# Performance work log

Hardware: AMD Instinct MI355X
Metric: run time of the kernel (lower is better)

The kernel has to match this reference:

```python
import jax, jax.numpy as jnp
import numpy as np

V, D, T, H, L, B = 50257, 1024, 1024, 16, 6, 2
HS = D // H  # 64
EPS = 1e-5


def setup_inputs() -> dict:
    key = jax.random.key(0)
    ks = jax.random.split(key, 16)
    s = 0.02
    n = lambda k, sh: jax.random.normal(k, sh, jnp.float32) * s
    return {
        'idx': jax.random.randint(ks[0], (B, T), 0, V),
        'targets': jax.random.randint(ks[1], (B, T), 0, V),
        'tok_emb': n(ks[2], (V, D)),
        'pos_emb': n(ks[3], (T, D)),
        'wq': n(ks[4], (L, H, D, HS)),
        'wk': n(ks[5], (L, H, D, HS)),
        'wv': n(ks[6], (L, H, D, HS)),
        'wproj': n(ks[7], (L, D, D)),
        'bproj': jnp.zeros((L, D), jnp.float32),
        'ln1_g': jnp.ones((L, D), jnp.float32),
        'ln1_b': jnp.zeros((L, D), jnp.float32),
        'ln2_g': jnp.ones((L, D), jnp.float32),
        'ln2_b': jnp.zeros((L, D), jnp.float32),
        'w1': n(ks[8], (L, D, 4 * D)),
        'b1': jnp.zeros((L, 4 * D), jnp.float32),
        'w2': n(ks[9], (L, 4 * D, D)),
        'b2': jnp.zeros((L, D), jnp.float32),
        'lnf_g': jnp.ones((D,), jnp.float32),
        'lnf_b': jnp.zeros((D,), jnp.float32),
        'lm_w': n(ks[10], (D, V)),
        'lm_b': jnp.zeros((V,), jnp.float32),
    }


def _layernorm(x, g, b):
    mu = jnp.mean(x, axis=-1, keepdims=True)
    var = jnp.var(x, axis=-1, keepdims=True)
    return (x - mu) * jax.lax.rsqrt(var + EPS) * g + b


def _forward(idx, targets, tok_emb, pos_emb, wq, wk, wv, wproj, bproj,
             ln1_g, ln1_b, ln2_g, ln2_b, w1, b1, w2, b2, lnf_g, lnf_b, lm_w, lm_b):
    t = idx.shape[1]
    x = tok_emb[idx] + pos_emb[:t]  # [B,T,D]
    causal = jnp.tril(jnp.ones((t, t), bool))  # [T,T]
    neg_inf = jnp.float32(-jnp.inf)

    def block(x, p):
        (wq_l, wk_l, wv_l, wp_l, bp_l, g1, b1_ln, g2, b2_ln, wf1, bf1, wf2, bf2) = p
        h = _layernorm(x, g1, b1_ln)
        q = jnp.einsum('btd,hdk->bhtk', h, wq_l)
        k = jnp.einsum('btd,hdk->bhtk', h, wk_l)
        v = jnp.einsum('btd,hdk->bhtk', h, wv_l)
        scores = jnp.einsum('bhtk,bhsk->bhts', q, k) * (HS ** -0.5)
        scores = jnp.where(causal, scores, neg_inf)
        attn = jax.nn.softmax(scores, axis=-1)  # dropout p=0.0
        o = jnp.einsum('bhts,bhsk->bhtk', attn, v)
        o = o.transpose(0, 2, 1, 3).reshape(x.shape[0], t, H * HS)  # concat heads
        x = x + o @ wp_l + bp_l
        h2 = _layernorm(x, g2, b2_ln)
        x = x + jax.nn.relu(h2 @ wf1 + bf1) @ wf2 + bf2
        return x, None

    x, _ = jax.lax.scan(block, x, (wq, wk, wv, wproj, bproj,
                                   ln1_g, ln1_b, ln2_g, ln2_b, w1, b1, w2, b2))
    x = _layernorm(x, lnf_g, lnf_b)
    logits = x @ lm_w + lm_b  # [B,T,V]
    logp = jax.nn.log_softmax(logits, axis=-1)
    loss = -jnp.mean(jnp.take_along_axis(logp, targets[..., None], axis=-1))
    return logits, loss


def reference(idx, targets, tok_emb, pos_emb, wq, wk, wv, wproj, bproj,
              ln1_g, ln1_b, ln2_g, ln2_b, w1, b1, w2, b2, lnf_g, lnf_b, lm_w, lm_b):
    return _forward(idx, targets, tok_emb, pos_emb, wq, wk, wv, wproj, bproj,
                    ln1_g, ln1_b, ln2_g, ln2_b, w1, b1, w2, b2, lnf_g, lnf_b, lm_w, lm_b)
```

## Files before the change

kernel.cpp:

```cpp
#include <hip/hip_runtime.h>
#include <cstdint>
#include <cstddef>

typedef unsigned short u16;
typedef unsigned int u32;
typedef __bf16 bf16x8 __attribute__((ext_vector_type(8)));
typedef float f32x4 __attribute__((ext_vector_type(4)));
typedef short short8_t __attribute__((ext_vector_type(8)));

#define NV 50257
#define NVPAD 50304
#define NBLK_LM 393
#define PSTR 400
#define ND 1024
#define NT 1024
#define NH 16
#define NL 6
#define NB 2
#define NM 2048
#define NF 4096
#define EPSLN 1e-5f

__device__ __forceinline__ u16 f2bf(float f) {
    unsigned u = __float_as_uint(f);
    return (u16)((u + 0x7fffu + ((u >> 16) & 1u)) >> 16);
}
__device__ __forceinline__ float bf2f(u16 h) {
    return __uint_as_float(((unsigned)h) << 16);
}
__device__ __forceinline__ u32 pack2bf(float lo, float hi) {
    return (u32)f2bf(lo) | ((u32)f2bf(hi) << 16);
}

__device__ __forceinline__ void gload_lds16(const u16* g, u16* l) {
    __builtin_amdgcn_global_load_lds((const __attribute__((address_space(1))) void*)g,
                                     (__attribute__((address_space(3))) void*)l, 16, 0, 0);
}

__device__ __forceinline__ float wave_reduce_sum(float v) {
#pragma unroll
    for (int off = 32; off >= 1; off >>= 1) v += __shfl_xor(v, off, 64);
    return v;
}

__global__ __launch_bounds__(256) void k_embed(const int* __restrict__ idx,
                                               const float* __restrict__ tok,
                                               const float* __restrict__ pos,
                                               float* __restrict__ x) {
    int m = blockIdx.x;
    int t = m & (NT - 1);
    int tokid = idx[m];
    int d = threadIdx.x * 4;
    float4 a = *(const float4*)(tok + (size_t)tokid * ND + d);
    float4 p = *(const float4*)(pos + (size_t)t * ND + d);
    a.x += p.x; a.y += p.y; a.z += p.z; a.w += p.w;
    *(float4*)(x + (size_t)m * ND + d) = a;
}

__global__ __launch_bounds__(256) void k_layernorm(const float* __restrict__ x,
                                                   const float* __restrict__ g,
                                                   const float* __restrict__ b,
                                                   u16* __restrict__ outb) {
    int m = blockIdx.x;
    int d = threadIdx.x * 4;
    const float4 v = *(const float4*)(x + (size_t)m * ND + d);
    float s = v.x + v.y + v.z + v.w;
    float q = v.x * v.x + v.y * v.y + v.z * v.z + v.w * v.w;
    s = wave_reduce_sum(s);
    q = wave_reduce_sum(q);
    __shared__ float ss[4], sq[4];
    int lane = threadIdx.x & 63, w = threadIdx.x >> 6;
    if (lane == 0) { ss[w] = s; sq[w] = q; }
    __syncthreads();
    s = ss[0] + ss[1] + ss[2] + ss[3];
    q = sq[0] + sq[1] + sq[2] + sq[3];
    float mu = s * (1.0f / ND);
    float var = q * (1.0f / ND) - mu * mu;
    float rstd = rsqrtf(var + EPSLN);
    float4 gg = *(const float4*)(g + d);
    float4 bb = *(const float4*)(b + d);
    ushort4 pk;
    pk.x = f2bf((v.x - mu) * rstd * gg.x + bb.x);
    pk.y = f2bf((v.y - mu) * rstd * gg.y + bb.y);
    pk.z = f2bf((v.z - mu) * rstd * gg.z + bb.z);
    pk.w = f2bf((v.w - mu) * rstd * gg.w + bb.w);
    *(ushort4*)(outb + (size_t)m * ND + d) = pk;
}

__global__ __launch_bounds__(256) void k_wtrans(const float* __restrict__ W,
                                                u16* __restrict__ Wt,
                                                int K, int N, int Npad, int hs, int ld) {
    __shared__ float t[32][33];
    const int nb = blockIdx.x << 5, kb = blockIdx.y << 5;
    const int tx = threadIdx.x & 31, tq = threadIdx.x >> 5;
    const int n = nb + tx;
    if (n < N) {
        const int head = n / hs, nc = n - head * hs;
        const float* src = W + (size_t)head * K * hs + nc;
#pragma unroll
        for (int i = 0; i < 4; ++i)
            t[(tq << 2) + i][tx] = src[(size_t)(kb + (tq << 2) + i) * ld];
    } else {
#pragma unroll
        for (int i = 0; i < 4; ++i) t[(tq << 2) + i][tx] = 0.f;
    }
    __syncthreads();
#pragma unroll
    for (int i = 0; i < 4; ++i) {
        const int nn = nb + (tq << 2) + i;
        if (nn < Npad) Wt[(size_t)nn * K + kb + tx] = f2bf(t[tx][(tq << 2) + i]);
    }
}

__global__ __launch_bounds__(256) void k_wtrans_qkv(const float* __restrict__ Wq,
                                                    const float* __restrict__ Wk,
                                                    const float* __restrict__ Wv,
                                                    u16* __restrict__ Wt) {
    __shared__ float t[32][33];
    const float* W = (blockIdx.z == 0) ? Wq : (blockIdx.z == 1) ? Wk : Wv;
    u16* dst = Wt + (size_t)blockIdx.z * ND * ND;
    const int nb = blockIdx.x << 5, kb = blockIdx.y << 5;
    const int tx = threadIdx.x & 31, tq = threadIdx.x >> 5;
    const int n = nb + tx;
    {
        const int head = n >> 6, nc = n & 63;
        const float* src = W + (size_t)head * ND * 64 + nc;
#pragma unroll
        for (int i = 0; i < 4; ++i)
            t[(tq << 2) + i][tx] = src[(size_t)(kb + (tq << 2) + i) * 64];
    }
    __syncthreads();
#pragma unroll
    for (int i = 0; i < 4; ++i) {
        const int nn = nb + (tq << 2) + i;
        dst[(size_t)nn * ND + kb + tx] = f2bf(t[tx][(tq << 2) + i]);
    }
}

__global__ __launch_bounds__(256) void k_vtrans(const u16* __restrict__ qkv,
                                                u16* __restrict__ vt) {
    __shared__ u16 L[64][72];
    const int tt = blockIdx.x, bh = blockIdx.y;
    const int b = bh >> 4, h = bh & 15;
    const int tid = threadIdx.x;
    const int tr = tid >> 2, dc = (tid & 3) << 4;
    const u16* src = qkv + (size_t)(b * NT + tt * 64 + tr) * 3072 + 2048 + h * 64 + dc;
    short8_t v0 = *(const short8_t*)src;
    short8_t v1 = *(const short8_t*)(src + 8);
#pragma unroll
    for (int j = 0; j < 8; ++j) { L[tr][dc + j] = (u16)v0[j]; L[tr][dc + 8 + j] = (u16)v1[j]; }
    __syncthreads();
    const int dr = tid >> 2, tc = (tid & 3) << 4;
    union { u16 us[16]; short8_t v[2]; } tmp;
#pragma unroll
    for (int j = 0; j < 16; ++j) tmp.us[j] = L[tc + j][dr];
    u16* dst = vt + ((size_t)bh * 64 + dr) * NT + tt * 64 + tc;
    *(short8_t*)dst = tmp.v[0];
    *(short8_t*)(dst + 8) = tmp.v[1];
}

template <bool RELU, bool RESID, bool NBOUND, bool PART, bool OUTBF16>
__global__ __launch_bounds__(256) void k_mfma_gemm(
    const u16* __restrict__ A, const u16* __restrict__ Bt,
    const float* __restrict__ bias, const float* __restrict__ resid,
    float* __restrict__ Cf, u16* __restrict__ Cb,
    float* __restrict__ pmax_g, float* __restrict__ psum_g,
    int K, int N, int ldc)
{
    __shared__ u16 As[2][128 * 32];
    __shared__ u16 Bs[2][128 * 32];
    const int lin = blockIdx.y * 16 + blockIdx.x;
    const int nwg = (int)gridDim.y * 16;
    const int cpx = nwg >> 3;
    const int swz = (lin & 7) * cpx + (lin >> 3);
    const int m0 = (swz & 15) * 128;
    const int n0 = (swz >> 4) * 128;
    const int tid = threadIdx.x;
    const int lane = tid & 63, wv = tid >> 6;
    const int wr = wv >> 1, wc = wv & 1;
    const int lr = lane & 15, kg = lane >> 4;

    const int srow = lane >> 2;
    const int scol = (((lane & 3) ^ ((lane >> 3) & 3)) << 3);
    const u16* gA0 = A + (size_t)(m0 + wv * 16 + srow) * K + scol;
    const u16* gA1 = gA0 + (size_t)64 * K;
    const u16* gB0 = Bt + (size_t)(n0 + wv * 16 + srow) * K + scol;
    const u16* gB1 = gB0 + (size_t)64 * K;

    f32x4 acc[4][4] = {};
    const int nt = K >> 5;

    gload_lds16(gA0, &As[0][wv * 512]);
    gload_lds16(gA1, &As[0][2048 + wv * 512]);
    gload_lds16(gB0, &Bs[0][wv * 512]);
    gload_lds16(gB1, &Bs[0][2048 + wv * 512]);
    __syncthreads();

    int cur = 0;
    for (int t = 0; t < nt; ++t) {
        if (t + 1 < nt) {
            const int ko = (t + 1) << 5;
            gload_lds16(gA0 + ko, &As[cur ^ 1][wv * 512]);
            gload_lds16(gA1 + ko, &As[cur ^ 1][2048 + wv * 512]);
            gload_lds16(gB0 + ko, &Bs[cur ^ 1][wv * 512]);
            gload_lds16(gB1 + ko, &Bs[cur ^ 1][2048 + wv * 512]);
        }
        bf16x8 af[4], bfr[4];
        const int rsw = ((kg ^ ((lr >> 1) & 3)) << 3);
#pragma unroll
        for (int mi = 0; mi < 4; ++mi) {
            const int R = wr * 64 + mi * 16 + lr;
            af[mi] = *(const bf16x8*)&As[cur][R * 32 + rsw];
        }
#pragma unroll
        for (int ni = 0; ni < 4; ++ni) {
            const int R = wc * 64 + ni * 16 + lr;
            bfr[ni] = *(const bf16x8*)&Bs[cur][R * 32 + rsw];
        }
#pragma unroll
        for (int mi = 0; mi < 4; ++mi)
#pragma unroll
            for (int ni = 0; ni < 4; ++ni)
                acc[mi][ni] = __builtin_amdgcn_mfma_f32_16x16x32_bf16(af[mi], bfr[ni], acc[mi][ni], 0, 0, 0);
        __syncthreads();
        cur ^= 1;
    }
#pragma unroll
    for (int mi = 0; mi < 4; ++mi) {
#pragma unroll
        for (int ni = 0; ni < 4; ++ni) {
#pragma unroll
            for (int r = 0; r < 4; ++r) {
                const int row = m0 + wr * 64 + mi * 16 + kg * 4 + r;
                const int col = n0 + wc * 64 + ni * 16 + lr;
                if (NBOUND && col >= N) continue;
                float c = acc[mi][ni][r];
                if (bias) c += bias[col];
                if (RELU) c = fmaxf(c, 0.f);
                if (RESID) c += resid[(size_t)row * ldc + col];
                if (OUTBF16) Cb[(size_t)row * ldc + col] = f2bf(c);
                else         Cf[(size_t)row * ldc + col] = c;
            }
        }
    }
    if constexpr (PART) {
        __shared__ float redm[128][2];
        __shared__ float reds[128][2];
#pragma unroll
        for (int mi = 0; mi < 4; ++mi)
#pragma unroll
            for (int r = 0; r < 4; ++r) {
                float vmax = -3.0e38f;
#pragma unroll
                for (int ni = 0; ni < 4; ++ni) {
                    const int col = n0 + wc * 64 + ni * 16 + lr;
                    float c = acc[mi][ni][r] + ((col < N) ? bias[col] : 0.f);
                    if (col >= N) c = -3.0e38f;
                    vmax = fmaxf(vmax, c);
                }
                vmax = fmaxf(vmax, __shfl_xor(vmax, 1));
                vmax = fmaxf(vmax, __shfl_xor(vmax, 2));
                vmax = fmaxf(vmax, __shfl_xor(vmax, 4));
                vmax = fmaxf(vmax, __shfl_xor(vmax, 8));
                if (lr == 0) redm[wr * 64 + mi * 16 + kg * 4 + r][wc] = vmax;
            }
        __syncthreads();
#pragma unroll
        for (int mi = 0; mi < 4; ++mi)
#pragma unroll
            for (int r = 0; r < 4; ++r) {
                const int rloc = wr * 64 + mi * 16 + kg * 4 + r;
                const float M = fmaxf(redm[rloc][0], redm[rloc][1]);
                float s = 0.f;
#pragma unroll
                for (int ni = 0; ni < 4; ++ni) {
                    const int col = n0 + wc * 64 + ni * 16 + lr;
                    if (col < N) {
                        float c = acc[mi][ni][r] + bias[col];
                        s += __expf(c - M);
                    }
                }
                s += __shfl_xor(s, 1);
                s += __shfl_xor(s, 2);
                s += __shfl_xor(s, 4);
                s += __shfl_xor(s, 8);
                if (lr == 0) reds[rloc][wc] = s;
            }
        __syncthreads();
        if (tid < 128) {
            const float M = fmaxf(redm[tid][0], redm[tid][1]);
            const int nblk = n0 >> 7;
            pmax_g[(size_t)(m0 + tid) * PSTR + nblk] = M;
            psum_g[(size_t)(m0 + tid) * PSTR + nblk] = reds[tid][0] + reds[tid][1];
        }
    }
}

template <bool RELU, bool RESID, bool OUTBF16>
__global__ __launch_bounds__(256) void k_gemm_n64(
    const u16* __restrict__ A, const u16* __restrict__ Bt,
    const float* __restrict__ bias, const float* __restrict__ resid,
    float* __restrict__ Cf, u16* __restrict__ Cb,
    int K, int ldc)
{
    __shared__ u16 As[2][128 * 32];
    __shared__ u16 Bs[2][64 * 32];
    const int lin = blockIdx.y * 16 + blockIdx.x;
    const int nwg = (int)gridDim.y * 16;
    const int cpx = nwg >> 3;
    const int swz = (lin & 7) * cpx + (lin >> 3);
    const int m0 = (swz & 15) * 128;
    const int n0 = (swz >> 4) * 64;
    const int tid = threadIdx.x;
    const int lane = tid & 63, wv = tid >> 6;
    const int lr = lane & 15, kg = lane >> 4;

    const int srow = lane >> 2;
    const int scol = (((lane & 3) ^ ((lane >> 3) & 3)) << 3);
    const u16* gA0 = A + (size_t)(m0 + wv * 32 + srow) * K + scol;
    const u16* gA1 = gA0 + (size_t)16 * K;
    const u16* gB0 = Bt + (size_t)(n0 + wv * 16 + srow) * K + scol;

    f32x4 acc[2][4] = {};
    const int nt = K >> 5;

    gload_lds16(gA0, &As[0][wv * 1024]);
    gload_lds16(gA1, &As[0][wv * 1024 + 512]);
    gload_lds16(gB0, &Bs[0][wv * 512]);
    __syncthreads();

    int cur = 0;
    for (int t = 0; t < nt; ++t) {
        if (t + 1 < nt) {
            const int ko = (t + 1) << 5;
            gload_lds16(gA0 + ko, &As[cur ^ 1][wv * 1024]);
            gload_lds16(gA1 + ko, &As[cur ^ 1][wv * 1024 + 512]);
            gload_lds16(gB0 + ko, &Bs[cur ^ 1][wv * 512]);
        }
        bf16x8 af[2], bfr[4];
        const int rsw = ((kg ^ ((lr >> 1) & 3)) << 3);
#pragma unroll
        for (int mi = 0; mi < 2; ++mi)
            af[mi] = *(const bf16x8*)&As[cur][(wv * 32 + mi * 16 + lr) * 32 + rsw];
#pragma unroll
        for (int ni = 0; ni < 4; ++ni)
            bfr[ni] = *(const bf16x8*)&Bs[cur][(ni * 16 + lr) * 32 + rsw];
#pragma unroll
        for (int mi = 0; mi < 2; ++mi)
#pragma unroll
            for (int ni = 0; ni < 4; ++ni)
                acc[mi][ni] = __builtin_amdgcn_mfma_f32_16x16x32_bf16(af[mi], bfr[ni], acc[mi][ni], 0, 0, 0);
        __syncthreads();
        cur ^= 1;
    }
#pragma unroll
    for (int mi = 0; mi < 2; ++mi) {
#pragma unroll
        for (int ni = 0; ni < 4; ++ni) {
#pragma unroll
            for (int r = 0; r < 4; ++r) {
                const int row = m0 + wv * 32 + mi * 16 + kg * 4 + r;
                const int col = n0 + ni * 16 + lr;
                float c = acc[mi][ni][r];
                if (bias) c += bias[col];
                if (RELU) c = fmaxf(c, 0.f);
                if (RESID) c += resid[(size_t)row * ldc + col];
                if (OUTBF16) Cb[(size_t)row * ldc + col] = f2bf(c);
                else         Cf[(size_t)row * ldc + col] = c;
            }
        }
    }
}

__global__ __launch_bounds__(256) void k_attn_mfma(const u16* __restrict__ qkv,
                                                   const u16* __restrict__ vt,
                                                   u16* __restrict__ ob) {
    const int qt = blockIdx.x, bh = blockIdx.y;
    const int b = bh >> 4, h = bh & 15;
    const int tid = threadIdx.x;
    const int lane = tid & 63, w = tid >> 6;
    const int lr = lane & 15, kg = lane >> 4;

    __shared__ u16 Qs[64 * 64];
    __shared__ u16 Ks[2][64 * 64];
    __shared__ u16 Vs[2][64 * 64];

    const int srow8 = lane >> 3;
    const int csw = ((lane & 7) ^ srow8) << 3;

    {
        const int r0 = w * 8 + srow8;
        gload_lds16(qkv + (size_t)(b * NT + qt * 64 + r0) * 3072 + h * 64 + csw, &Qs[w * 512]);
        gload_lds16(qkv + (size_t)(b * NT + qt * 64 + 32 + r0) * 3072 + h * 64 + csw, &Qs[2048 + w * 512]);
    }
#define STAGE_KV(bb, st)                                                                            \
    {                                                                                               \
        const int r0_ = w * 8 + srow8;                                                              \
        gload_lds16(qkv + (size_t)(b * NT + (st) * 64 + r0_) * 3072 + 1024 + h * 64 + csw,          \
                    &Ks[bb][w * 512]);                                                              \
        gload_lds16(qkv + (size_t)(b * NT + (st) * 64 + 32 + r0_) * 3072 + 1024 + h * 64 + csw,     \
                    &Ks[bb][2048 + w * 512]);                                                       \
        gload_lds16(vt + ((size_t)bh * 64 + r0_) * NT + (st) * 64 + csw, &Vs[bb][w * 512]);         \
        gload_lds16(vt + ((size_t)bh * 64 + 32 + r0_) * NT + (st) * 64 + csw,                       \
                    &Vs[bb][2048 + w * 512]);                                                       \
    }
    STAGE_KV(0, 0);
    __syncthreads();

    bf16x8 qf[2];
    {
        const int qrow = w * 16 + lr;
#pragma unroll
        for (int ds_ = 0; ds_ < 2; ++ds_)
            qf[ds_] = *(const bf16x8*)&Qs[qrow * 64 + ((((ds_ << 2) + kg) ^ (lr & 7)) << 3)];
    }

    float mstate = -3.0e38f, lstate = 0.f;
    f32x4 acc_o[4] = {};
    const int qg = qt * 64 + w * 16 + lr;

    int cur = 0;
    for (int st = 0; st <= qt; ++st) {
        if (st < qt) STAGE_KV(cur ^ 1, st + 1);
        const bool diag = (st == qt);
        const int milim = diag ? w : 3;

        f32x4 acc_s[4] = {};
#pragma unroll
        for (int mi = 0; mi < 4; ++mi) {
            if (mi <= milim) {
                const int srw = mi * 16 + lr;
#pragma unroll
                for (int ds_ = 0; ds_ < 2; ++ds_) {
                    bf16x8 kf = *(const bf16x8*)&Ks[cur][srw * 64 + ((((ds_ << 2) + kg) ^ (lr & 7)) << 3)];
                    acc_s[mi] = __builtin_amdgcn_mfma_f32_16x16x32_bf16(kf, qf[ds_], acc_s[mi], 0, 0, 0);
                }
            }
        }
        float tilemax = -3.0e38f;
#pragma unroll
        for (int mi = 0; mi < 4; ++mi)
#pragma unroll
            for (int r = 0; r < 4; ++r) {
                float x_ = acc_s[mi][r] * 0.125f;
                const int sg = st * 64 + mi * 16 + kg * 4 + r;
                if (mi > milim || sg > qg) x_ = -3.0e38f;
                acc_s[mi][r] = x_;
                tilemax = fmaxf(tilemax, x_);
            }
        tilemax = fmaxf(tilemax, __shfl_xor(tilemax, 16));
        tilemax = fmaxf(tilemax, __shfl_xor(tilemax, 32));
        const float mnew = fmaxf(mstate, tilemax);
        const float rfac = __expf(mstate - mnew);
        mstate = mnew;

        float psum = 0.f;
        u32 pk[4][2];
#pragma unroll
        for (int mi = 0; mi < 4; ++mi) {
            float p0 = __expf(acc_s[mi][0] - mnew);
            float p1 = __expf(acc_s[mi][1] - mnew);
            float p2 = __expf(acc_s[mi][2] - mnew);
            float p3 = __expf(acc_s[mi][3] - mnew);
            psum += p0 + p1 + p2 + p3;
            pk[mi][0] = pack2bf(p0, p1);
            pk[mi][1] = pack2bf(p2, p3);
        }
        psum += __shfl_xor(psum, 16);
        psum += __shfl_xor(psum, 32);
        lstate = lstate * rfac + psum;

        float rf[4];
#pragma unroll
        for (int r = 0; r < 4; ++r) rf[r] = __shfl(rfac, kg * 4 + r);
#pragma unroll
        for (int ni = 0; ni < 4; ++ni)
#pragma unroll
            for (int r = 0; r < 4; ++r) acc_o[ni][r] *= rf[r];

        const int src0 = ((kg & 1) << 5) + lr;
        const int src1 = src0 + 16;
#pragma unroll
        for (int ks_ = 0; ks_ < 2; ++ks_) {
            const u32 lo_a = __shfl((int)pk[ks_ * 2][0], src0);
            const u32 lo_b = __shfl((int)pk[ks_ * 2][1], src0);
            const u32 lo_c = __shfl((int)pk[ks_ * 2][0], src1);
            const u32 lo_d = __shfl((int)pk[ks_ * 2][1], src1);
            const u32 hi_a = __shfl((int)pk[ks_ * 2 + 1][0], src0);
            const u32 hi_b = __shfl((int)pk[ks_ * 2 + 1][1], src0);
            const u32 hi_c = __shfl((int)pk[ks_ * 2 + 1][0], src1);
            const u32 hi_d = __shfl((int)pk[ks_ * 2 + 1][1], src1);
            union { u32 u[4]; bf16x8 v; } pa;
            pa.u[0] = (kg & 2) ? hi_a : lo_a;
            pa.u[1] = (kg & 2) ? hi_b : lo_b;
            pa.u[2] = (kg & 2) ? hi_c : lo_c;
            pa.u[3] = (kg & 2) ? hi_d : lo_d;
#pragma unroll
            for (int ni = 0; ni < 4; ++ni) {
                const int drow = ni * 16 + lr;
                bf16x8 vf = *(const bf16x8*)&Vs[cur][drow * 64 + ((((ks_ << 2) + kg) ^ (lr & 7)) << 3)];
                acc_o[ni] = __builtin_amdgcn_mfma_f32_16x16x32_bf16(pa.v, vf, acc_o[ni], 0, 0, 0);
            }
        }
        __syncthreads();
        cur ^= 1;
    }

    float il[4];
#pragma unroll
    for (int r = 0; r < 4; ++r) il[r] = 1.0f / __shfl(lstate, kg * 4 + r);
#pragma unroll
    for (int ni = 0; ni < 4; ++ni)
#pragma unroll
        for (int r = 0; r < 4; ++r) {
            const int q2 = qt * 64 + w * 16 + kg * 4 + r;
            ob[(size_t)(b * NT + q2) * ND + h * 64 + ni * 16 + lr] = f2bf(acc_o[ni][r] * il[r]);
        }
#undef STAGE_KV
}

__global__ __launch_bounds__(256) void k_losscombine(const float* __restrict__ pmax,
                                                     const float* __restrict__ psum,
                                                     const float* __restrict__ logits,
                                                     const int* __restrict__ targets,
                                                     float* __restrict__ rl) {
    const int row = blockIdx.x * 4 + (threadIdx.x >> 6);
    const int lane = threadIdx.x & 63;
    const float* pm = pmax + (size_t)row * PSTR;
    const float* ps = psum + (size_t)row * PSTR;
    float M = -3.0e38f;
    for (int j = lane; j < NBLK_LM; j += 64) M = fmaxf(M, pm[j]);
#pragma unroll
    for (int off = 32; off >= 1; off >>= 1) M = fmaxf(M, __shfl_xor(M, off, 64));
    float S = 0.f;
    for (int j = lane; j < NBLK_LM; j += 64) S += ps[j] * __expf(pm[j] - M);
    S = wave_reduce_sum(S);
    if (lane == 0)
        rl[row] = M + logf(S) - logits[(size_t)row * NV + targets[row]];
}

__global__ __launch_bounds__(256) void k_lossreduce(const float* __restrict__ rl,
                                                    float* __restrict__ out_loss) {
    int tid = threadIdx.x;
    float s = 0.f;
    for (int j = tid; j < NM; j += 256) s += rl[j];
    s = wave_reduce_sum(s);
    __shared__ float sv[4];
    int lane = tid & 63, w = tid >> 6;
    if (lane == 0) sv[w] = s;
    __syncthreads();
    if (tid == 0) out_loss[0] = (sv[0] + sv[1] + sv[2] + sv[3]) * (1.0f / NM);
}

extern "C" void kernel_launch(void* const* d_in, const int* in_sizes, int n_in,
                              void* d_out, int out_size, void* d_ws, size_t ws_size,
                              hipStream_t stream) {
    const int* idx      = (const int*)d_in[0];
    const int* targets  = (const int*)d_in[1];
    const float* tok    = (const float*)d_in[2];
    const float* pos    = (const float*)d_in[3];
    const float* wq     = (const float*)d_in[4];
    const float* wk     = (const float*)d_in[5];
    const float* wv     = (const float*)d_in[6];
    const float* wproj  = (const float*)d_in[7];
    const float* bproj  = (const float*)d_in[8];
    const float* ln1_g  = (const float*)d_in[9];
    const float* ln1_b  = (const float*)d_in[10];
    const float* ln2_g  = (const float*)d_in[11];
    const float* ln2_b  = (const float*)d_in[12];
    const float* w1     = (const float*)d_in[13];
    const float* b1     = (const float*)d_in[14];
    const float* w2     = (const float*)d_in[15];
    const float* b2     = (const float*)d_in[16];
    const float* lnf_g  = (const float*)d_in[17];
    const float* lnf_b  = (const float*)d_in[18];
    const float* lm_w   = (const float*)d_in[19];
    const float* lm_b   = (const float*)d_in[20];
    float* out = (float*)d_out;

    char* wsb = (char*)d_ws;
    auto alloc = [&](size_t bytes) { char* p = wsb; wsb += (bytes + 255) & ~(size_t)255; return p; };
    float* x     = (float*)alloc((size_t)NM * ND * 4);
    u16* h_bf    = (u16*)  alloc((size_t)NM * ND * 2);
    float* rl    = (float*)alloc((size_t)NM * 4);
    float* pmax  = (float*)alloc((size_t)NM * PSTR * 4);
    float* psum  = (float*)alloc((size_t)NM * PSTR * 4);
    char* region = (char*)alloc((size_t)NVPAD * ND * 2);
    u16* qkv_bf = (u16*)(region);
    u16* vt_bf  = (u16*)(region + ((size_t)12 << 20));
    u16* ob_bf  = (u16*)(region + ((size_t)16 << 20));
    u16* hid_bf = (u16*)(region + ((size_t)20 << 20));
    u16* wqkv_t = (u16*)(region + ((size_t)36 << 20));
    u16* wp_t   = (u16*)(region + ((size_t)42 << 20));
    u16* w1_t   = (u16*)(region + ((size_t)44 << 20));
    u16* w2_t   = (u16*)(region + ((size_t)52 << 20));
    u16* lm_t   = (u16*)(region);

    k_embed<<<NM, 256, 0, stream>>>(idx, tok, pos, x);

    for (int l = 0; l < NL; ++l) {
        const float* wq_l = wq + (size_t)l * NH * ND * 64;
        const float* wk_l = wk + (size_t)l * NH * ND * 64;
        const float* wv_l = wv + (size_t)l * NH * ND * 64;
        const float* wp_l = wproj + (size_t)l * ND * ND;
        const float* bp_l = bproj + (size_t)l * ND;
        const float* w1_l = w1 + (size_t)l * ND * NF;
        const float* b1_l = b1 + (size_t)l * NF;
        const float* w2_l = w2 + (size_t)l * NF * ND;
        const float* b2_l = b2 + (size_t)l * ND;

        k_layernorm<<<NM, 256, 0, stream>>>(x, ln1_g + (size_t)l * ND, ln1_b + (size_t)l * ND, h_bf);

        k_wtrans_qkv<<<dim3(32, 32, 3), 256, 0, stream>>>(wq_l, wk_l, wv_l, wqkv_t);
        k_mfma_gemm<false, false, false, false, true><<<dim3(16, 24), 256, 0, stream>>>(
            h_bf, wqkv_t, nullptr, nullptr, nullptr, qkv_bf, nullptr, nullptr, ND, 3 * ND, 3 * ND);

        k_vtrans<<<dim3(NT / 64, NB * NH), 256, 0, stream>>>(qkv_bf, vt_bf);
        k_attn_mfma<<<dim3(NT / 64, NB * NH), 256, 0, stream>>>(qkv_bf, vt_bf, ob_bf);

        k_wtrans<<<dim3(ND / 32, ND / 32), 256, 0, stream>>>(wp_l, wp_t, ND, ND, ND, ND, ND);
        k_gemm_n64<false, true, false><<<dim3(16, 16), 256, 0, stream>>>(
            ob_bf, wp_t, bp_l, x, x, nullptr, ND, ND);

        k_layernorm<<<NM, 256, 0, stream>>>(x, ln2_g + (size_t)l * ND, ln2_b + (size_t)l * ND, h_bf);

        k_wtrans<<<dim3(NF / 32, ND / 32), 256, 0, stream>>>(w1_l, w1_t, ND, NF, NF, NF, NF);
        k_mfma_gemm<true, false, false, false, true><<<dim3(16, 32), 256, 0, stream>>>(
            h_bf, w1_t, b1_l, nullptr, nullptr, hid_bf, nullptr, nullptr, ND, NF, NF);

        k_wtrans<<<dim3(ND / 32, NF / 32), 256, 0, stream>>>(w2_l, w2_t, NF, ND, ND, ND, ND);
        k_gemm_n64<false, true, false><<<dim3(16, 16), 256, 0, stream>>>(
            hid_bf, w2_t, b2_l, x, x, nullptr, NF, ND);
    }

    k_layernorm<<<NM, 256, 0, stream>>>(x, lnf_g, lnf_b, h_bf);

    k_wtrans<<<dim3(NVPAD / 32, ND / 32), 256, 0, stream>>>(lm_w, lm_t, ND, NV, NVPAD, NV, NV);
    k_mfma_gemm<false, false, true, true, false><<<dim3(16, NVPAD / 128), 256, 0, stream>>>(
        h_bf, lm_t, lm_b, nullptr, out, nullptr, pmax, psum, ND, NV, NV);

    k_losscombine<<<NM / 4, 256, 0, stream>>>(pmax, psum, out, targets, rl);
    k_lossreduce<<<1, 256, 0, stream>>>(rl, out + (size_t)NM * NV);
}
```

Measured before the change: 1.948 ms.

## Unfuse LM-head partial softmax stats into a separate row-wise loss kernel

Drops the per-tile max/sum-exp epilogue from the LM-head GEMM, along with its partial-stat buffers and the combine kernel. Adds a row-wise loss kernel that re-reads each full logits row (about 200KB per row) with float4 loads to compute the log-sum-exp and the target loss. This makes the GEMM epilogue lighter and removes its extra syncthreads, but adds a second pass over the roughly 400MB logits tensor, so the loss step becomes memory-bound. The unused RESID template path is also removed.

```diff
diff --git a/kernel.cpp b/kernel.cpp
--- a/kernel.cpp
+++ b/kernel.cpp
@@ -10,8 +10,6 @@
 
 #define NV 50257
 #define NVPAD 50304
-#define NBLK_LM 393
-#define PSTR 400
 #define ND 1024
 #define NT 1024
 #define NH 16
@@ -159,12 +157,11 @@
     *(short8_t*)(dst + 8) = tmp.v[1];
 }
 
-template <bool RELU, bool RESID, bool NBOUND, bool PART, bool OUTBF16>
+template <bool RELU, bool NBOUND, bool OUTBF16>
 __global__ __launch_bounds__(256) void k_mfma_gemm(
     const u16* __restrict__ A, const u16* __restrict__ Bt,
-    const float* __restrict__ bias, const float* __restrict__ resid,
+    const float* __restrict__ bias,
     float* __restrict__ Cf, u16* __restrict__ Cb,
-    float* __restrict__ pmax_g, float* __restrict__ psum_g,
     int K, int N, int ldc)
 {
     __shared__ u16 As[2][128 * 32];
@@ -237,61 +234,9 @@
                 float c = acc[mi][ni][r];
                 if (bias) c += bias[col];
                 if (RELU) c = fmaxf(c, 0.f);
-                if (RESID) c += resid[(size_t)row * ldc + col];
                 if (OUTBF16) Cb[(size_t)row * ldc + col] = f2bf(c);
                 else         Cf[(size_t)row * ldc + col] = c;
             }
-        }
-    }
-    if constexpr (PART) {
-        __shared__ float redm[128][2];
-        __shared__ float reds[128][2];
-#pragma unroll
-        for (int mi = 0; mi < 4; ++mi)
-#pragma unroll
-            for (int r = 0; r < 4; ++r) {
-                float vmax = -3.0e38f;
-#pragma unroll
-                for (int ni = 0; ni < 4; ++ni) {
-                    const int col = n0 + wc * 64 + ni * 16 + lr;
-                    float c = acc[mi][ni][r] + ((col < N) ? bias[col] : 0.f);
-                    if (col >= N) c = -3.0e38f;
-                    vmax = fmaxf(vmax, c);
-                }
-                vmax = fmaxf(vmax, __shfl_xor(vmax, 1));
-                vmax = fmaxf(vmax, __shfl_xor(vmax, 2));
-                vmax = fmaxf(vmax, __shfl_xor(vmax, 4));
-                vmax = fmaxf(vmax, __shfl_xor(vmax, 8));
-                if (lr == 0) redm[wr * 64 + mi * 16 + kg * 4 + r][wc] = vmax;
-            }
-        __syncthreads();
-#pragma unroll
-        for (int mi = 0; mi < 4; ++mi)
-#pragma unroll
-            for (int r = 0; r < 4; ++r) {
-                const int rloc = wr * 64 + mi * 16 + kg * 4 + r;
-                const float M = fmaxf(redm[rloc][0], redm[rloc][1]);
-                float s = 0.f;
-#pragma unroll
-                for (int ni = 0; ni < 4; ++ni) {
-                    const int col = n0 + wc * 64 + ni * 16 + lr;
-                    if (col < N) {
-                        float c = acc[mi][ni][r] + bias[col];
-                        s += __expf(c - M);
-                    }
-                }
-                s += __shfl_xor(s, 1);
-                s += __shfl_xor(s, 2);
-                s += __shfl_xor(s, 4);
-                s += __shfl_xor(s, 8);
-                if (lr == 0) reds[rloc][wc] = s;
-            }
-        __syncthreads();
-        if (tid < 128) {
-            const float M = fmaxf(redm[tid][0], redm[tid][1]);
-            const int nblk = n0 >> 7;
-            pmax_g[(size_t)(m0 + tid) * PSTR + nblk] = M;
-            psum_g[(size_t)(m0 + tid) * PSTR + nblk] = reds[tid][0] + reds[tid][1];
         }
     }
 }
@@ -519,24 +464,48 @@
 #undef STAGE_KV
 }
 
-__global__ __launch_bounds__(256) void k_losscombine(const float* __restrict__ pmax,
-                                                     const float* __restrict__ psum,
-                                                     const float* __restrict__ logits,
-                                                     const int* __restrict__ targets,
-                                                     float* __restrict__ rl) {
-    const int row = blockIdx.x * 4 + (threadIdx.x >> 6);
-    const int lane = threadIdx.x & 63;
-    const float* pm = pmax + (size_t)row * PSTR;
-    const float* ps = psum + (size_t)row * PSTR;
-    float M = -3.0e38f;
-    for (int j = lane; j < NBLK_LM; j += 64) M = fmaxf(M, pm[j]);
-#pragma unroll
-    for (int off = 32; off >= 1; off >>= 1) M = fmaxf(M, __shfl_xor(M, off, 64));
-    float S = 0.f;
-    for (int j = lane; j < NBLK_LM; j += 64) S += ps[j] * __expf(pm[j] - M);
-    S = wave_reduce_sum(S);
-    if (lane == 0)
-        rl[row] = M + logf(S) - logits[(size_t)row * NV + targets[row]];
+__global__ __launch_bounds__(256) void k_rowloss(const float* __restrict__ logits,
+                                                 const int* __restrict__ targets,
+                                                 float* __restrict__ rl) {
+    const int m = blockIdx.x;
+    const float* row = logits + (size_t)m * NV;
+    const int tid = threadIdx.x;
+    const int lane = tid & 63, w = tid >> 6;
+    const int a = (4 - (m & 3)) & 3;
+    const float4* rv = (const float4*)(row + a);
+    const int nv4 = (NV - a) >> 2;
+    const int tail0 = a + (nv4 << 2);
+
+    float mx = -INFINITY;
+    if (tid < a) mx = row[tid];
+    for (int j = tid; j < nv4; j += 256) {
+        float4 v = rv[j];
+        mx = fmaxf(fmaxf(mx, v.x), fmaxf(v.y, fmaxf(v.z, v.w)));
+    }
+    for (int j = tail0 + tid; j < NV; j += 256) mx = fmaxf(mx, row[j]);
+#pragma unroll
+    for (int off = 32; off >= 1; off >>= 1) mx = fmaxf(mx, __shfl_xor(mx, off, 64));
+    __shared__ float sm[4];
+    if (lane == 0) sm[w] = mx;
+    __syncthreads();
+    mx = fmaxf(fmaxf(sm[0], sm[1]), fmaxf(sm[2], sm[3]));
+
+    float s = 0.f;
+    if (tid < a) s += __expf(row[tid] - mx);
+    for (int j = tid; j < nv4; j += 256) {
+        float4 v = rv[j];
+        s += __expf(v.x - mx) + __expf(v.y - mx) + __expf(v.z - mx) + __expf(v.w - mx);
+    }
+    for (int j = tail0 + tid; j < NV; j += 256) s += __expf(row[j] - mx);
+    s = wave_reduce_sum(s);
+    __shared__ float sv[4];
+    if (lane == 0) sv[w] = s;
+    __syncthreads();
+    s = sv[0] + sv[1] + sv[2] + sv[3];
+    if (tid == 0) {
+        float lse = logf(s) + mx;
+        rl[m] = lse - row[targets[m]];
+    }
 }
 
 __global__ __launch_bounds__(256) void k_lossreduce(const float* __restrict__ rl,
@@ -583,8 +552,6 @@
     float* x     = (float*)alloc((size_t)NM * ND * 4);
     u16* h_bf    = (u16*)  alloc((size_t)NM * ND * 2);
     float* rl    = (float*)alloc((size_t)NM * 4);
-    float* pmax  = (float*)alloc((size_t)NM * PSTR * 4);
-    float* psum  = (float*)alloc((size_t)NM * PSTR * 4);
     char* region = (char*)alloc((size_t)NVPAD * ND * 2);
     u16* qkv_bf = (u16*)(region);
     u16* vt_bf  = (u16*)(region + ((size_t)12 << 20));
@@ -612,8 +579,8 @@
         k_layernorm<<<NM, 256, 0, stream>>>(x, ln1_g + (size_t)l * ND, ln1_b + (size_t)l * ND, h_bf);
 
         k_wtrans_qkv<<<dim3(32, 32, 3), 256, 0, stream>>>(wq_l, wk_l, wv_l, wqkv_t);
-        k_mfma_gemm<false, false, false, false, true><<<dim3(16, 24), 256, 0, stream>>>(
-            h_bf, wqkv_t, nullptr, nullptr, nullptr, qkv_bf, nullptr, nullptr, ND, 3 * ND, 3 * ND);
+        k_mfma_gemm<false, false, true><<<dim3(16, 24), 256, 0, stream>>>(
+            h_bf, wqkv_t, nullptr, nullptr, qkv_bf, ND, 3 * ND, 3 * ND);
 
         k_vtrans<<<dim3(NT / 64, NB * NH), 256, 0, stream>>>(qkv_bf, vt_bf);
         k_attn_mfma<<<dim3(NT / 64, NB * NH), 256, 0, stream>>>(qkv_bf, vt_bf, ob_bf);
@@ -625,8 +592,8 @@
         k_layernorm<<<NM, 256, 0, stream>>>(x, ln2_g + (size_t)l * ND, ln2_b + (size_t)l * ND, h_bf);
 
         k_wtrans<<<dim3(NF / 32, ND / 32), 256, 0, stream>>>(w1_l, w1_t, ND, NF, NF, NF, NF);
-        k_mfma_gemm<true, false, false, false, true><<<dim3(16, 32), 256, 0, stream>>>(
-            h_bf, w1_t, b1_l, nullptr, nullptr, hid_bf, nullptr, nullptr, ND, NF, NF);
+        k_mfma_gemm<true, false, true><<<dim3(16, 32), 256, 0, stream>>>(
+            h_bf, w1_t, b1_l, nullptr, hid_bf, ND, NF, NF);
 
         k_wtrans<<<dim3(ND / 32, NF / 32), 256, 0, stream>>>(w2_l, w2_t, NF, ND, ND, ND, ND);
         k_gemm_n64<false, true, false><<<dim3(16, 16), 256, 0, stream>>>(
@@ -636,9 +603,9 @@
     k_layernorm<<<NM, 256, 0, stream>>>(x, lnf_g, lnf_b, h_bf);
 
     k_wtrans<<<dim3(NVPAD / 32, ND / 32), 256, 0, stream>>>(lm_w, lm_t, ND, NV, NVPAD, NV, NV);
-    k_mfma_gemm<false, false, true, true, false><<<dim3(16, NVPAD / 128), 256, 0, stream>>>(
-        h_bf, lm_t, lm_b, nullptr, out, nullptr, pmax, psum, ND, NV, NV);
-
-    k_losscombine<<<NM / 4, 256, 0, stream>>>(pmax, psum, out, targets, rl);
+    k_mfma_gemm<false, true, false><<<dim3(16, NVPAD / 128), 256, 0, stream>>>(
+        h_bf, lm_t, lm_b, out, nullptr, ND, NV, NV);
+
+    k_rowloss<<<NM, 256, 0, stream>>>(out, targets, rl);
     k_lossreduce<<<1, 256, 0, stream>>>(rl, out + (size_t)NM * NV);
 }
```

Result: no change. 1.963 ms (+0.8%).
